# Kernel tuning notes

Hardware: AMD Instinct MI355X
Metric: run time of the kernel (lower is better)

The kernel has to match this reference:

```python
import jax, jax.numpy as jnp
import numpy as np

HEADS = 16
ROPE_BASE = 10000.0


def _rope(x):
    # x: [b, h, n, d]. lucidrains partial rotary: RotaryEmbedding(head_dim//2)
    # rotates only the first rot_dim = d//2 channels, interleaved-pair style.
    d = x.shape[-1]
    rot = d // 2
    inv_freq = 1.0 / (ROPE_BASE ** (jnp.arange(0, rot, 2, dtype=jnp.float32) / rot))  # [rot//2]
    pos = jnp.arange(x.shape[2], dtype=jnp.float32)
    freqs = pos[:, None] * inv_freq[None, :]                  # [n, rot//2]
    cos, sin = jnp.cos(freqs), jnp.sin(freqs)
    xr, xp = x[..., :rot], x[..., rot:]
    x1, x2 = xr[..., 0::2], xr[..., 1::2]                     # interleaved pairs
    o1 = x1 * cos - x2 * sin
    o2 = x2 * cos + x1 * sin
    xr_out = jnp.stack([o1, o2], axis=-1).reshape(xr.shape)   # re-interleave
    return jnp.concatenate([xr_out, xp], axis=-1)


def setup_inputs() -> dict:
    key = jax.random.key(0)
    k0, k1 = jax.random.split(key)
    B, N, D = 2, 2048, 2048
    x = jax.random.normal(k0, (B, N, D), dtype=jnp.float32)
    W_qkv = jax.random.normal(k1, (3 * D, D), dtype=jnp.float32) * (D ** -0.5)
    b_qkv = jnp.zeros((3 * D,), dtype=jnp.float32)
    return {"x": x, "W_qkv": W_qkv, "b_qkv": b_qkv}


def reference(x, W_qkv, b_qkv):
    B, N, D = x.shape
    H = HEADS
    hd = D // H
    qkv = x @ W_qkv.T + b_qkv                                  # [b, n, 3d]
    q, k, v = jnp.split(qkv, 3, axis=-1)
    to_heads = lambda t: t.reshape(B, N, H, hd).transpose(0, 2, 1, 3)  # b h n d
    q, k, v = to_heads(q), to_heads(k), to_heads(v)
    q, k = _rope(q), _rope(k)
    scale = 1.0 / np.sqrt(hd)
    scores = jnp.einsum('bhnd,bhmd->bhnm', q, k) * scale
    causal = jnp.tril(jnp.ones((N, N), dtype=bool))
    scores = jnp.where(causal, scores, -jnp.inf)
    attn = jax.nn.softmax(scores, axis=-1)
    y = jnp.einsum('bhnm,bhmd->bhnd', attn, v)
    return y.transpose(0, 2, 1, 3).reshape(B, N, D)
```

## Files before the change

kernel.cpp:

```cpp
#include <hip/hip_runtime.h>
#include <hip/hip_bf16.h>
#include <math.h>

typedef unsigned short u16;
typedef unsigned int u32;
typedef __attribute__((ext_vector_type(8))) short bf16x8;
typedef __attribute__((ext_vector_type(4))) float f32x4;

#define B_ 2
#define N_ 2048
#define D_ 2048
#define H_ 16
#define HD 128
#define GK 2048

__device__ __forceinline__ u16 f2bf(float f) {
  u32 u = __float_as_uint(f);
  u = (u + 0x7fffu + ((u >> 16) & 1u)) >> 16;
  return (u16)u;
}

__device__ __forceinline__ u32 cvtpk(float lo, float hi) {
  u32 r;
  asm("v_cvt_pk_bf16_f32 %0, %1, %2" : "=v"(r) : "v"(lo), "v"(hi));
  return r;
}

__device__ __forceinline__ void gload_lds16(const void* g, void* l) {
  __builtin_amdgcn_global_load_lds(
      (const __attribute__((address_space(1))) u32*)g,
      (__attribute__((address_space(3))) u32*)l, 16, 0, 0);
}

__global__ __launch_bounds__(256) void cvt_kernel(const float* __restrict__ in,
                                                  u16* __restrict__ out, int n4) {
  int i = blockIdx.x * blockDim.x + threadIdx.x;
  int st = gridDim.x * blockDim.x;
  for (; i < n4; i += st) {
    float4 v = ((const float4*)in)[i];
    ushort4 o;
    o.x = f2bf(v.x); o.y = f2bf(v.y); o.z = f2bf(v.z); o.w = f2bf(v.w);
    ((ushort4*)out)[i] = o;
  }
}

__global__ __launch_bounds__(256) void rope_tbl_kernel(float* __restrict__ tbl) {
  int i = blockIdx.x * blockDim.x + threadIdx.x;
  if (i >= N_ * 32) return;
  int pos = i >> 5, p = i & 31;
  double inv = pow(10000.0, -(double)p / 32.0);
  double a = (double)pos * inv;
  tbl[2 * i]     = (float)cos(a);
  tbl[2 * i + 1] = (float)sin(a);
}

__global__ __launch_bounds__(512, 2) void qkv_gemm_kernel(
    const u16* __restrict__ X, const u16* __restrict__ W,
    const float* __restrict__ bias, const float* __restrict__ tbl,
    u16* __restrict__ Qo, u16* __restrict__ Ko, u16* __restrict__ Vo) {
  __shared__ char smem[147456];
  const int tid = threadIdx.x;
  const int lane = tid & 63;
  const int w = tid >> 6;
  const int wm = w >> 2, wn = w & 3;
  const int l15 = lane & 15, l4 = lane >> 4;

  const int bid = blockIdx.x;
  const int wg = (bid & 7) * 64 + (bid >> 3);
  const int n0 = (wg & 31) * 192;
  const int m0 = (wg >> 5) * 256;

  const int aof0 = (l4 * 16) ^ ((l15 & 7) << 4);
  const int aof1 = (64 + l4 * 16) ^ ((l15 & 7) << 4);
  const int kfA = wm ? aof1 : aof0;
  const int ksA = wm ? aof0 : aof1;

  int srowA[2], scolA[2];
#pragma unroll
  for (int p = 0; p < 2; ++p) {
    int o = (w * 2 + p) * 1024 + lane * 16;
    int lo = o ^ (((o >> 7) & 7) << 4);
    srowA[p] = lo >> 7;
    scolA[p] = (lo & 127) >> 1;
  }
  const int oB = w * 1024 + lane * 16;
  const int loB = oB ^ (((oB >> 7) & 7) << 4);
  const int srowB = loB >> 7, scolB = (loB & 127) >> 1;

  f32x4 acc[8][3];
#pragma unroll
  for (int fm = 0; fm < 8; ++fm)
#pragma unroll
    for (int fn = 0; fn < 3; ++fn)
#pragma unroll
      for (int q = 0; q < 4; ++q) acc[fm][fn][q] = 0.f;

  auto stageA = [&](char* Abase, int half, int k0) {
#pragma unroll
    for (int p = 0; p < 2; ++p) {
      gload_lds16(X + (size_t)(m0 + half * 128 + srowA[p]) * GK + k0 + scolA[p],
                  Abase + half * 16384 + (w * 2 + p) * 1024);
    }
  };
  auto stageB = [&](char* Bbase, int chunk, int k0) {
    gload_lds16(W + (size_t)(n0 + chunk * 64 + srowB) * GK + k0 + scolB,
                Bbase + chunk * 8192 + w * 1024);
  };

  const int NK = GK / 64;

  stageA(smem, 0, 0); stageA(smem, 1, 0);
  stageB(smem + 98304, 0, 0); stageB(smem + 98304, 1, 0); stageB(smem + 98304, 2, 0);
  stageA(smem + 32768, 0, 64); stageA(smem + 32768, 1, 64);
  asm volatile("s_waitcnt vmcnt(4)" ::: "memory");
  __builtin_amdgcn_s_barrier();

  int at = 0;
  for (int T = 0; T < NK; ++T) {
    const int bt = T & 1;
    int an2 = at + 2; if (an2 >= 3) an2 -= 3;
    const char* Ab = smem + at * 32768 + wm * 16384;
    const char* Bb = smem + 98304 + bt * 24576;
    char* Bn = smem + 98304 + (bt ^ 1) * 24576;
    char* An = smem + an2 * 32768;
    const int kn1 = (T + 1) * 64, kn2 = (T + 2) * 64;
    const bool hasB = (T + 1 < NK), hasA = (T + 2 < NK);

    bf16x8 bf_[3], bs_[3], aq[4];

#pragma unroll
    for (int fn = 0; fn < 3; ++fn)
      bf_[fn] = *(const bf16x8*)(Bb + (wn * 48 + fn * 16 + l15) * 128 + kfA);
#pragma unroll
    for (int fm = 0; fm < 4; ++fm)
      aq[fm] = *(const bf16x8*)(Ab + (fm * 16 + l15) * 128 + kfA);
    if (hasB) { stageB(Bn, 0, kn1); stageB(Bn, 1, kn1); stageB(Bn, 2, kn1); }
    __builtin_amdgcn_s_setprio(1);
#pragma unroll
    for (int fm = 0; fm < 4; ++fm)
#pragma unroll
      for (int fn = 0; fn < 3; ++fn)
        acc[fm][fn] = __builtin_amdgcn_mfma_f32_16x16x32_bf16(aq[fm], bf_[fn], acc[fm][fn], 0, 0, 0);
    __builtin_amdgcn_s_setprio(0);

#pragma unroll
    for (int fm = 0; fm < 4; ++fm)
      aq[fm] = *(const bf16x8*)(Ab + ((fm + 4) * 16 + l15) * 128 + kfA);
    __builtin_amdgcn_s_setprio(1);
#pragma unroll
    for (int fm = 0; fm < 4; ++fm)
#pragma unroll
      for (int fn = 0; fn < 3; ++fn)
        acc[fm + 4][fn] = __builtin_amdgcn_mfma_f32_16x16x32_bf16(aq[fm], bf_[fn], acc[fm + 4][fn], 0, 0, 0);
    __builtin_amdgcn_s_setprio(0);

#pragma unroll
    for (int fn = 0; fn < 3; ++fn)
      bs_[fn] = *(const bf16x8*)(Bb + (wn * 48 + fn * 16 + l15) * 128 + ksA);
#pragma unroll
    for (int fm = 0; fm < 4; ++fm)
      aq[fm] = *(const bf16x8*)(Ab + (fm * 16 + l15) * 128 + ksA);
    if (hasA) { stageA(An, 0, kn2); stageA(An, 1, kn2); }
    __builtin_amdgcn_s_setprio(1);
#pragma unroll
    for (int fm = 0; fm < 4; ++fm)
#pragma unroll
      for (int fn = 0; fn < 3; ++fn)
        acc[fm][fn] = __builtin_amdgcn_mfma_f32_16x16x32_bf16(aq[fm], bs_[fn], acc[fm][fn], 0, 0, 0);
    __builtin_amdgcn_s_setprio(0);

#pragma unroll
    for (int fm = 0; fm < 4; ++fm)
      aq[fm] = *(const bf16x8*)(Ab + ((fm + 4) * 16 + l15) * 128 + ksA);
    if (hasA) {
      asm volatile("s_waitcnt vmcnt(4)" ::: "memory");
    } else {
      asm volatile("s_waitcnt vmcnt(0)" ::: "memory");
    }
    __builtin_amdgcn_s_setprio(1);
#pragma unroll
    for (int fm = 0; fm < 4; ++fm)
#pragma unroll
      for (int fn = 0; fn < 3; ++fn)
        acc[fm + 4][fn] = __builtin_amdgcn_mfma_f32_16x16x32_bf16(aq[fm], bs_[fn], acc[fm + 4][fn], 0, 0, 0);
    __builtin_amdgcn_s_setprio(0);
    __builtin_amdgcn_s_barrier();

    at = (at + 1 == 3) ? 0 : at + 1;
  }

  const float QSCALE = 0.08838834764831845f;
#pragma unroll
  for (int fn = 0; fn < 3; ++fn) {
    int gn = n0 + wn * 48 + fn * 16 + l15;
    float bv = bias[gn];
    int sec = gn >> 11;
    int wi = gn & 2047;
    int h = wi >> 7;
    int d = wi & 127;
    u16* dstbase = (sec == 0) ? Qo : (sec == 1) ? Ko : Vo;
    float mulf = (sec == 0) ? QSCALE : 1.f;
    bool doRope = (sec < 2) && (d < 64);
    int pidx = d >> 1;
    bool odd = (d & 1) != 0;
#pragma unroll
    for (int fm = 0; fm < 8; ++fm) {
#pragma unroll
      for (int j = 0; j < 4; ++j) {
        int gm = m0 + wm * 128 + fm * 16 + l4 * 4 + j;
        int bb = gm >> 11;
        int pos = gm & 2047;
        float v = acc[fm][fn][j] + bv;
        float pr = __shfl_xor(v, 1);
        float ov = v;
        if (doRope) {
          float2 cs = ((const float2*)tbl)[pos * 32 + pidx];
          ov = odd ? (v * cs.x + pr * cs.y) : (v * cs.x - pr * cs.y);
        }
        dstbase[(size_t)((bb * H_ + h) * N_ + pos) * HD + d] = f2bf(ov * mulf);
      }
    }
  }
}

__global__ __launch_bounds__(256, 2) void flash_kernel(
    const u16* __restrict__ Q, const u16* __restrict__ K, const u16* __restrict__ V,
    float* __restrict__ Out) {
  __shared__ char smem[69632];

  const int tid = threadIdx.x, lane = tid & 63, w = tid >> 6;
  const int l15 = lane & 15, l4 = lane >> 4;

  const int bid = blockIdx.x;
  const int xcd = bid & 7, slot = bid >> 3;
  const int bh = xcd * 4 + (slot >> 4);
  const int x = 15 - (slot & 15);
  const int bb = bh >> 4, h = bh & 15;
  const size_t base = (size_t)bh * (N_ * HD);
  const int q0 = x * 128;
  const int nt = 2 * x + 2;

  bf16x8 qf[2][4];
#pragma unroll
  for (int g = 0; g < 2; ++g) {
    const u16* qp = Q + base + (size_t)(q0 + w * 32 + g * 16 + l15) * HD + l4 * 8;
#pragma unroll
    for (int kf = 0; kf < 4; ++kf) qf[g][kf] = *(const bf16x8*)(qp + kf * 32);
  }

  float m_r[2] = {-1e30f, -1e30f}, l_r[2] = {0.f, 0.f};
  f32x4 accO[2][8];
#pragma unroll
  for (int g = 0; g < 2; ++g)
#pragma unroll
    for (int df = 0; df < 8; ++df)
#pragma unroll
      for (int q = 0; q < 4; ++q) accO[g][df][q] = 0.f;

  auto stageK = [&](int buf, int t0) {
    const u16* kb = K + base + (size_t)t0 * HD;
    char* kt = smem + buf * 16384;
#pragma unroll
    for (int i = 0; i < 4; ++i) {
      int c = w * 4 + i;
      int o = c * 1024 + lane * 16;
      int lo = o ^ (((o >> 8) & 7) << 4);
      gload_lds16(kb + (lo >> 1), kt + c * 1024);
    }
  };
  auto loadV = [&](int t0, bf16x8* vr) {
    const u16* vp = V + base + (size_t)(t0 + lane) * HD + w * 32;
#pragma unroll
    for (int i = 0; i < 4; ++i) vr[i] = *(const bf16x8*)(vp + i * 8);
  };
  auto writeV = [&](int buf, const bf16x8* vr) {
    u16* vt = (u16*)(smem + 32768 + buf * 18432);
#pragma unroll
    for (int i = 0; i < 4; ++i)
#pragma unroll
      for (int jj = 0; jj < 8; ++jj)
        vt[(w * 32 + i * 8 + jj) * 72 + lane] = (u16)vr[i][jj];
  };

  const int src0 = l15 + 32 * (l4 & 1);
  const int src1 = src0 + 16;
  const int half = l4 >> 1;
  union U8 { u32 u[4]; bf16x8 v; };

  bf16x8 vreg[4];
  stageK(0, 0);
  loadV(0, vreg);
  writeV(0, vreg);
  __syncthreads();

  for (int t = 0; t < nt; ++t) {
    const int cur = t & 1;
    const int t0 = t * 64;
    const bool pre = (t + 1 < nt);
    if (pre) { stageK(cur ^ 1, t0 + 64); loadV(t0 + 64, vreg); }

    const char* kt = smem + cur * 16384;
    const u16* vt = (const u16*)(smem + 32768 + cur * 18432);

    f32x4 s[2][4];
#pragma unroll
    for (int cf = 0; cf < 4; ++cf) {
#pragma unroll
      for (int q = 0; q < 4; ++q) { s[0][cf][q] = 0.f; s[1][cf][q] = 0.f; }
      int row = cf * 16 + l15;
      int sw = (row & 7) << 4;
#pragma unroll
      for (int kf = 0; kf < 4; ++kf) {
        int off = (row * 256 + kf * 64 + l4 * 16) ^ sw;
        bf16x8 kfrag = *(const bf16x8*)(kt + off);
        s[0][cf] = __builtin_amdgcn_mfma_f32_16x16x32_bf16(kfrag, qf[0][kf], s[0][cf], 0, 0, 0);
        s[1][cf] = __builtin_amdgcn_mfma_f32_16x16x32_bf16(kfrag, qf[1][kf], s[1][cf], 0, 0, 0);
      }
    }

    u32 pk[2][4][2];
#pragma unroll
    for (int g = 0; g < 2; ++g) {
      const int qbase = q0 + w * 32 + g * 16;
      if (t0 + 63 > qbase) {
        const int qg = qbase + l15;
#pragma unroll
        for (int cf = 0; cf < 4; ++cf)
#pragma unroll
          for (int j = 0; j < 4; ++j) {
            int kvg = t0 + cf * 16 + l4 * 4 + j;
            if (kvg > qg) s[g][cf][j] = -1e30f;
          }
      }
      float pmax = s[g][0][0];
#pragma unroll
      for (int cf = 0; cf < 4; ++cf)
#pragma unroll
        for (int j = 0; j < 4; ++j) pmax = fmaxf(pmax, s[g][cf][j]);
      pmax = fmaxf(pmax, __shfl_xor(pmax, 16));
      pmax = fmaxf(pmax, __shfl_xor(pmax, 32));

      if (!__all(pmax <= m_r[g] + 8.f)) {
        float mn = fmaxf(m_r[g], pmax);
        float rs = __expf(m_r[g] - mn);
        m_r[g] = mn;
        l_r[g] *= rs;
#pragma unroll
        for (int df = 0; df < 8; ++df)
#pragma unroll
          for (int j = 0; j < 4; ++j) accO[g][df][j] *= rs;
      }

      float ps = 0.f;
#pragma unroll
      for (int cf = 0; cf < 4; ++cf) {
        float p0 = __expf(s[g][cf][0] - m_r[g]);
        float p1 = __expf(s[g][cf][1] - m_r[g]);
        float p2 = __expf(s[g][cf][2] - m_r[g]);
        float p3 = __expf(s[g][cf][3] - m_r[g]);
        ps += (p0 + p1) + (p2 + p3);
        pk[g][cf][0] = cvtpk(p0, p1);
        pk[g][cf][1] = cvtpk(p2, p3);
      }
      ps += __shfl_xor(ps, 16);
      ps += __shfl_xor(ps, 32);
      l_r[g] += ps;
    }

#pragma unroll
    for (int c = 0; c < 2; ++c) {
      const int c2 = 2 * c;
      U8 pu[2];
#pragma unroll
      for (int g = 0; g < 2; ++g) {
        u32 a0 = (u32)__shfl((int)pk[g][c2][0], src0);
        u32 b0 = (u32)__shfl((int)pk[g][c2 + 1][0], src0);
        u32 a1 = (u32)__shfl((int)pk[g][c2][1], src0);
        u32 b1 = (u32)__shfl((int)pk[g][c2 + 1][1], src0);
        u32 a2 = (u32)__shfl((int)pk[g][c2][0], src1);
        u32 b2 = (u32)__shfl((int)pk[g][c2 + 1][0], src1);
        u32 a3 = (u32)__shfl((int)pk[g][c2][1], src1);
        u32 b3 = (u32)__shfl((int)pk[g][c2 + 1][1], src1);
        pu[g].u[0] = half ? b0 : a0;
        pu[g].u[1] = half ? b1 : a1;
        pu[g].u[2] = half ? b2 : a2;
        pu[g].u[3] = half ? b3 : a3;
      }
#pragma unroll
      for (int df = 0; df < 8; ++df) {
        bf16x8 vf = *(const bf16x8*)(vt + (df * 16 + l15) * 72 + c * 32 + l4 * 8);
        accO[0][df] = __builtin_amdgcn_mfma_f32_16x16x32_bf16(vf, pu[0].v, accO[0][df], 0, 0, 0);
        accO[1][df] = __builtin_amdgcn_mfma_f32_16x16x32_bf16(vf, pu[1].v, accO[1][df], 0, 0, 0);
      }
    }

    if (pre) writeV(cur ^ 1, vreg);
    __syncthreads();
  }

  float* Obuf = (float*)(smem + w * 8448);
  const int l31 = lane & 31;
#pragma unroll
  for (int g = 0; g < 2; ++g) {
    float inv = 1.f / l_r[g];
#pragma unroll
    for (int df = 0; df < 8; ++df) {
      f32x4 v = accO[g][df];
#pragma unroll
      for (int j = 0; j < 4; ++j) v[j] *= inv;
      *(f32x4*)&Obuf[l15 * 132 + df * 16 + l4 * 4] = v;
    }
#pragma unroll
    for (int p = 0; p < 8; ++p) {
      int row = p * 2 + (lane >> 5);
      f32x4 v = *(const f32x4*)&Obuf[row * 132 + l31 * 4];
      int qg = q0 + w * 32 + g * 16 + row;
      *(f32x4*)&Out[(size_t)(bb * N_ + qg) * D_ + h * HD + l31 * 4] = v;
    }
  }
}

extern "C" void kernel_launch(void* const* d_in, const int* in_sizes, int n_in,
                              void* d_out, int out_size, void* d_ws, size_t ws_size,
                              hipStream_t stream) {
  const float* x  = (const float*)d_in[0];
  const float* Wq = (const float*)d_in[1];
  const float* bq = (const float*)d_in[2];
  float* out = (float*)d_out;
  char* ws = (char*)d_ws;

  u16* Qb  = (u16*)(ws);
  u16* Kb  = (u16*)(ws + 16777216);
  u16* Vb  = (u16*)(ws + 2 * 16777216);
  u16* Xb  = (u16*)(ws + 3 * 16777216);
  u16* Wb  = (u16*)(ws + 4 * 16777216);
  float* tbl = (float*)(ws + 4 * 16777216 + 25165824);

  cvt_kernel<<<2048, 256, 0, stream>>>(x, Xb, (B_ * N_ * D_) / 4);
  cvt_kernel<<<2048, 256, 0, stream>>>(Wq, Wb, (3 * D_ * D_) / 4);
  rope_tbl_kernel<<<(N_ * 32 + 255) / 256, 256, 0, stream>>>(tbl);
  qkv_gemm_kernel<<<512, 512, 0, stream>>>(Xb, Wb, bq, tbl, Qb, Kb, Vb);
  flash_kernel<<<512, 256, 0, stream>>>(Qb, Kb, Vb, out);
}
```

Before: 252.1 us.

## Halve flash attention query tile to 64 rows and single-buffer V in LDS

The flash kernel now processes 64 query rows per block (16 per wave) instead of 128, doubling the grid to 1024 blocks and remapping block IDs so each XCD handles four heads with heavy tiles first. V staging in shared memory drops from double to single buffering, which shrinks LDS to 51200 bytes and adds an extra barrier before each V write. The aim is better load balance across CUs and lower register and LDS pressure. The cost is that each K/V tile is now loaded by twice as many blocks, and the added barrier serialises the V write with compute.

```diff
diff --git a/kernel.cpp b/kernel.cpp
--- a/kernel.cpp
+++ b/kernel.cpp
@@ -226,36 +226,33 @@
 __global__ __launch_bounds__(256, 2) void flash_kernel(
     const u16* __restrict__ Q, const u16* __restrict__ K, const u16* __restrict__ V,
     float* __restrict__ Out) {
-  __shared__ char smem[69632];
+  __shared__ char smem[51200];
 
   const int tid = threadIdx.x, lane = tid & 63, w = tid >> 6;
   const int l15 = lane & 15, l4 = lane >> 4;
 
   const int bid = blockIdx.x;
-  const int xcd = bid & 7, slot = bid >> 3;
-  const int bh = xcd * 4 + (slot >> 4);
-  const int x = 15 - (slot & 15);
+  const int xcd = bid & 7, s_ = bid >> 3;
+  const int bh = xcd * 4 + (s_ & 3);
+  const int x = 31 - (s_ >> 2);
   const int bb = bh >> 4, h = bh & 15;
   const size_t base = (size_t)bh * (N_ * HD);
-  const int q0 = x * 128;
-  const int nt = 2 * x + 2;
-
-  bf16x8 qf[2][4];
-#pragma unroll
-  for (int g = 0; g < 2; ++g) {
-    const u16* qp = Q + base + (size_t)(q0 + w * 32 + g * 16 + l15) * HD + l4 * 8;
-#pragma unroll
-    for (int kf = 0; kf < 4; ++kf) qf[g][kf] = *(const bf16x8*)(qp + kf * 32);
-  }
-
-  float m_r[2] = {-1e30f, -1e30f}, l_r[2] = {0.f, 0.f};
-  f32x4 accO[2][8];
-#pragma unroll
-  for (int g = 0; g < 2; ++g)
-#pragma unroll
-    for (int df = 0; df < 8; ++df)
-#pragma unroll
-      for (int q = 0; q < 4; ++q) accO[g][df][q] = 0.f;
+  const int q0 = x * 64;
+  const int nt = x + 1;
+
+  bf16x8 qf[4];
+  {
+    const u16* qp = Q + base + (size_t)(q0 + w * 16 + l15) * HD + l4 * 8;
+#pragma unroll
+    for (int kf = 0; kf < 4; ++kf) qf[kf] = *(const bf16x8*)(qp + kf * 32);
+  }
+
+  float m_r = -1e30f, l_r = 0.f;
+  f32x4 accO[8];
+#pragma unroll
+  for (int df = 0; df < 8; ++df)
+#pragma unroll
+    for (int q = 0; q < 4; ++q) accO[df][q] = 0.f;
 
   auto stageK = [&](int buf, int t0) {
     const u16* kb = K + base + (size_t)t0 * HD;
@@ -273,8 +270,8 @@
 #pragma unroll
     for (int i = 0; i < 4; ++i) vr[i] = *(const bf16x8*)(vp + i * 8);
   };
-  auto writeV = [&](int buf, const bf16x8* vr) {
-    u16* vt = (u16*)(smem + 32768 + buf * 18432);
+  auto writeV = [&](const bf16x8* vr) {
+    u16* vt = (u16*)(smem + 32768);
 #pragma unroll
     for (int i = 0; i < 4; ++i)
 #pragma unroll
@@ -290,7 +287,8 @@
   bf16x8 vreg[4];
   stageK(0, 0);
   loadV(0, vreg);
-  writeV(0, vreg);
+  __syncthreads();
+  writeV(vreg);
   __syncthreads();
 
   for (int t = 0; t < nt; ++t) {
@@ -300,123 +298,116 @@
     if (pre) { stageK(cur ^ 1, t0 + 64); loadV(t0 + 64, vreg); }
 
     const char* kt = smem + cur * 16384;
-    const u16* vt = (const u16*)(smem + 32768 + cur * 18432);
-
-    f32x4 s[2][4];
+    const u16* vt = (const u16*)(smem + 32768);
+
+    f32x4 s[4];
 #pragma unroll
     for (int cf = 0; cf < 4; ++cf) {
 #pragma unroll
-      for (int q = 0; q < 4; ++q) { s[0][cf][q] = 0.f; s[1][cf][q] = 0.f; }
+      for (int q = 0; q < 4; ++q) s[cf][q] = 0.f;
       int row = cf * 16 + l15;
       int sw = (row & 7) << 4;
 #pragma unroll
       for (int kf = 0; kf < 4; ++kf) {
         int off = (row * 256 + kf * 64 + l4 * 16) ^ sw;
         bf16x8 kfrag = *(const bf16x8*)(kt + off);
-        s[0][cf] = __builtin_amdgcn_mfma_f32_16x16x32_bf16(kfrag, qf[0][kf], s[0][cf], 0, 0, 0);
-        s[1][cf] = __builtin_amdgcn_mfma_f32_16x16x32_bf16(kfrag, qf[1][kf], s[1][cf], 0, 0, 0);
+        s[cf] = __builtin_amdgcn_mfma_f32_16x16x32_bf16(kfrag, qf[kf], s[cf], 0, 0, 0);
       }
     }
 
-    u32 pk[2][4][2];
-#pragma unroll
-    for (int g = 0; g < 2; ++g) {
-      const int qbase = q0 + w * 32 + g * 16;
-      if (t0 + 63 > qbase) {
-        const int qg = qbase + l15;
-#pragma unroll
-        for (int cf = 0; cf < 4; ++cf)
-#pragma unroll
-          for (int j = 0; j < 4; ++j) {
-            int kvg = t0 + cf * 16 + l4 * 4 + j;
-            if (kvg > qg) s[g][cf][j] = -1e30f;
-          }
-      }
-      float pmax = s[g][0][0];
+    const int qbase = q0 + w * 16;
+    if (t0 + 63 > qbase) {
+      const int qg = qbase + l15;
 #pragma unroll
       for (int cf = 0; cf < 4; ++cf)
 #pragma unroll
-        for (int j = 0; j < 4; ++j) pmax = fmaxf(pmax, s[g][cf][j]);
-      pmax = fmaxf(pmax, __shfl_xor(pmax, 16));
-      pmax = fmaxf(pmax, __shfl_xor(pmax, 32));
-
-      if (!__all(pmax <= m_r[g] + 8.f)) {
-        float mn = fmaxf(m_r[g], pmax);
-        float rs = __expf(m_r[g] - mn);
-        m_r[g] = mn;
-        l_r[g] *= rs;
-#pragma unroll
-        for (int df = 0; df < 8; ++df)
-#pragma unroll
-          for (int j = 0; j < 4; ++j) accO[g][df][j] *= rs;
-      }
-
-      float ps = 0.f;
-#pragma unroll
-      for (int cf = 0; cf < 4; ++cf) {
-        float p0 = __expf(s[g][cf][0] - m_r[g]);
-        float p1 = __expf(s[g][cf][1] - m_r[g]);
-        float p2 = __expf(s[g][cf][2] - m_r[g]);
-        float p3 = __expf(s[g][cf][3] - m_r[g]);
-        ps += (p0 + p1) + (p2 + p3);
-        pk[g][cf][0] = cvtpk(p0, p1);
-        pk[g][cf][1] = cvtpk(p2, p3);
-      }
-      ps += __shfl_xor(ps, 16);
-      ps += __shfl_xor(ps, 32);
-      l_r[g] += ps;
-    }
+        for (int j = 0; j < 4; ++j) {
+          int kvg = t0 + cf * 16 + l4 * 4 + j;
+          if (kvg > qg) s[cf][j] = -1e30f;
+        }
+    }
+
+    float pmax = s[0][0];
+#pragma unroll
+    for (int cf = 0; cf < 4; ++cf)
+#pragma unroll
+      for (int j = 0; j < 4; ++j) pmax = fmaxf(pmax, s[cf][j]);
+    pmax = fmaxf(pmax, __shfl_xor(pmax, 16));
+    pmax = fmaxf(pmax, __shfl_xor(pmax, 32));
+
+    if (!__all(pmax <= m_r + 8.f)) {
+      float mn = fmaxf(m_r, pmax);
+      float rs = __expf(m_r - mn);
+      m_r = mn;
+      l_r *= rs;
+#pragma unroll
+      for (int df = 0; df < 8; ++df)
+#pragma unroll
+        for (int j = 0; j < 4; ++j) accO[df][j] *= rs;
+    }
+
+    u32 pk[4][2];
+    float ps = 0.f;
+#pragma unroll
+    for (int cf = 0; cf < 4; ++cf) {
+      float p0 = __expf(s[cf][0] - m_r);
+      float p1 = __expf(s[cf][1] - m_r);
+      float p2 = __expf(s[cf][2] - m_r);
+      float p3 = __expf(s[cf][3] - m_r);
+      ps += (p0 + p1) + (p2 + p3);
+      pk[cf][0] = cvtpk(p0, p1);
+      pk[cf][1] = cvtpk(p2, p3);
+    }
+    ps += __shfl_xor(ps, 16);
+    ps += __shfl_xor(ps, 32);
+    l_r += ps;
 
 #pragma unroll
     for (int c = 0; c < 2; ++c) {
       const int c2 = 2 * c;
-      U8 pu[2];
-#pragma unroll
-      for (int g = 0; g < 2; ++g) {
-        u32 a0 = (u32)__shfl((int)pk[g][c2][0], src0);
-        u32 b0 = (u32)__shfl((int)pk[g][c2 + 1][0], src0);
-        u32 a1 = (u32)__shfl((int)pk[g][c2][1], src0);
-        u32 b1 = (u32)__shfl((int)pk[g][c2 + 1][1], src0);
-        u32 a2 = (u32)__shfl((int)pk[g][c2][0], src1);
-        u32 b2 = (u32)__shfl((int)pk[g][c2 + 1][0], src1);
-        u32 a3 = (u32)__shfl((int)pk[g][c2][1], src1);
-        u32 b3 = (u32)__shfl((int)pk[g][c2 + 1][1], src1);
-        pu[g].u[0] = half ? b0 : a0;
-        pu[g].u[1] = half ? b1 : a1;
-        pu[g].u[2] = half ? b2 : a2;
-        pu[g].u[3] = half ? b3 : a3;
-      }
+      u32 a0 = (u32)__shfl((int)pk[c2][0], src0);
+      u32 b0 = (u32)__shfl((int)pk[c2 + 1][0], src0);
+      u32 a1 = (u32)__shfl((int)pk[c2][1], src0);
+      u32 b1 = (u32)__shfl((int)pk[c2 + 1][1], src0);
+      u32 a2 = (u32)__shfl((int)pk[c2][0], src1);
+      u32 b2 = (u32)__shfl((int)pk[c2 + 1][0], src1);
+      u32 a3 = (u32)__shfl((int)pk[c2][1], src1);
+      u32 b3 = (u32)__shfl((int)pk[c2 + 1][1], src1);
+      U8 pu;
+      pu.u[0] = half ? b0 : a0;
+      pu.u[1] = half ? b1 : a1;
+      pu.u[2] = half ? b2 : a2;
+      pu.u[3] = half ? b3 : a3;
 #pragma unroll
       for (int df = 0; df < 8; ++df) {
         bf16x8 vf = *(const bf16x8*)(vt + (df * 16 + l15) * 72 + c * 32 + l4 * 8);
-        accO[0][df] = __builtin_amdgcn_mfma_f32_16x16x32_bf16(vf, pu[0].v, accO[0][df], 0, 0, 0);
-        accO[1][df] = __builtin_amdgcn_mfma_f32_16x16x32_bf16(vf, pu[1].v, accO[1][df], 0, 0, 0);
+        accO[df] = __builtin_amdgcn_mfma_f32_16x16x32_bf16(vf, pu.v, accO[df], 0, 0, 0);
       }
     }
 
-    if (pre) writeV(cur ^ 1, vreg);
+    __syncthreads();
+    if (pre) writeV(vreg);
     __syncthreads();
   }
 
   float* Obuf = (float*)(smem + w * 8448);
   const int l31 = lane & 31;
-#pragma unroll
-  for (int g = 0; g < 2; ++g) {
-    float inv = 1.f / l_r[g];
+  {
+    float inv = 1.f / l_r;
 #pragma unroll
     for (int df = 0; df < 8; ++df) {
-      f32x4 v = accO[g][df];
+      f32x4 v = accO[df];
 #pragma unroll
       for (int j = 0; j < 4; ++j) v[j] *= inv;
       *(f32x4*)&Obuf[l15 * 132 + df * 16 + l4 * 4] = v;
     }
-#pragma unroll
-    for (int p = 0; p < 8; ++p) {
-      int row = p * 2 + (lane >> 5);
-      f32x4 v = *(const f32x4*)&Obuf[row * 132 + l31 * 4];
-      int qg = q0 + w * 32 + g * 16 + row;
-      *(f32x4*)&Out[(size_t)(bb * N_ + qg) * D_ + h * HD + l31 * 4] = v;
-    }
+  }
+#pragma unroll
+  for (int p = 0; p < 8; ++p) {
+    int row = p * 2 + (lane >> 5);
+    f32x4 v = *(const f32x4*)&Obuf[row * 132 + l31 * 4];
+    int qg = q0 + w * 16 + row;
+    *(f32x4*)&Out[(size_t)(bb * N_ + qg) * D_ + h * HD + l31 * 4] = v;
   }
 }
 
@@ -440,5 +431,5 @@
   cvt_kernel<<<2048, 256, 0, stream>>>(Wq, Wb, (3 * D_ * D_) / 4);
   rope_tbl_kernel<<<(N_ * 32 + 255) / 256, 256, 0, stream>>>(tbl);
   qkv_gemm_kernel<<<512, 512, 0, stream>>>(Xb, Wb, bq, tbl, Qb, Kb, Vb);
-  flash_kernel<<<512, 256, 0, stream>>>(Qb, Kb, Vb, out);
-}
+  flash_kernel<<<1024, 256, 0, stream>>>(Qb, Kb, Vb, out);
+}
```

After: 233.0 us. -7.6%, faster.
